# Optimization experiments

Measured on AMD Instinct MI355X. Metric: run time of the kernel, lower is better.

The kernel has to match this reference:

```python
import jax, jax.numpy as jnp
import numpy as np

B, S, D, H = 2, 4096, 512, 8
HD = D // H


def setup_inputs() -> dict:
    key = jax.random.key(0)
    ks = jax.random.split(key, 11)
    s = 1.0 / np.sqrt(D)
    return {
        "queries": jax.random.normal(ks[0], (B, S, D), jnp.float32),
        "keys": jax.random.normal(ks[1], (B, S, D), jnp.float32),
        "values": jax.random.normal(ks[2], (B, S, D), jnp.float32),
        "Wq": jax.random.normal(ks[3], (D, D), jnp.float32) * s,
        "bq": jnp.zeros((D,), jnp.float32),
        "Wk": jax.random.normal(ks[4], (D, D), jnp.float32) * s,
        "bk": jnp.zeros((D,), jnp.float32),
        "Wv": jax.random.normal(ks[5], (D, D), jnp.float32) * s,
        "bv": jnp.zeros((D,), jnp.float32),
        "Wo": jax.random.normal(ks[6], (D, D), jnp.float32) * s,
        "bo": jnp.zeros((D,), jnp.float32),
    }


def reference(queries, keys, values, Wq, bq, Wk, bk, Wv, bv, Wo, bo):
    b = queries.shape[0]
    # Linear projections (torch Linear: x @ W.T + b; here W stored as [in, out])
    q = (queries @ Wq + bq).reshape(b, -1, H, HD)   # [B, Sq, H, HD]
    k = (keys @ Wk + bk).reshape(b, -1, H, HD)       # [B, Sk, H, HD]
    v = (values @ Wv + bv).reshape(b, -1, H, HD)     # [B, Sk, H, HD]
    logits = jnp.einsum('bqhd,bkhd->bhqk', q, k) / jnp.sqrt(jnp.float32(HD))
    attn = jax.nn.softmax(logits, axis=-1)           # [B, H, Sq, Sk]  (dropout_rate=0 -> identity)
    ctx = jnp.einsum('bhqk,bkhd->bqhd', attn, v).reshape(b, -1, H * HD)
    return ctx @ Wo + bo
```

## Files before the change

### kernel.cpp

```cpp
#include <hip/hip_runtime.h>
#include <hip/hip_bf16.h>

constexpr int B_  = 2;
constexpr int S_  = 4096;
constexpr int D_  = 512;
constexpr int H_  = 8;
constexpr int HD_ = 64;
constexpr int M_  = B_ * S_;

typedef __attribute__((ext_vector_type(8))) short short8;
typedef __attribute__((ext_vector_type(4))) float floatx4;
typedef __attribute__((ext_vector_type(16))) float floatx16;

static __device__ __forceinline__ unsigned short f2bf(float f) {
    union { float f; unsigned u; } v; v.f = f;
    unsigned r = v.u + 0x7fffu + ((v.u >> 16) & 1u);
    return (unsigned short)(r >> 16);
}

static __device__ __forceinline__ unsigned pk2bf(float a, float b) {
#if __has_builtin(__builtin_amdgcn_cvt_pk_bf16_f32)
    typedef __attribute__((ext_vector_type(2))) __bf16 bf16x2_t;
    union { bf16x2_t v; unsigned u; } u;
    u.v = __builtin_amdgcn_cvt_pk_bf16_f32(a, b);
    return u.u;
#else
    return (unsigned)f2bf(a) | ((unsigned)f2bf(b) << 16);
#endif
}

static __device__ __forceinline__ void plane32swap(unsigned& x, unsigned& y) {
#if __has_builtin(__builtin_amdgcn_permlane32_swap)
    typedef __attribute__((ext_vector_type(2))) unsigned uint2v;
    uint2v r = __builtin_amdgcn_permlane32_swap(x, y, false, false);
    x = r[0]; y = r[1];
#else
    const bool hi = (threadIdx.x & 32) != 0;
    unsigned xs = __shfl_xor(x, 32), ys = __shfl_xor(y, 32);
    unsigned nx = hi ? ys : x;
    unsigned ny = hi ? y : xs;
    x = nx; y = ny;
#endif
}

#if __has_builtin(__builtin_amdgcn_exp2f)
#define EXP2(x) __builtin_amdgcn_exp2f(x)
#else
#define EXP2(x) exp2f(x)
#endif

#define QSCALE 0.18033688011110204f

static __device__ __forceinline__ void gl_lds16(const void* g, void* l) {
    typedef __attribute__((address_space(1))) const unsigned GU;
    typedef __attribute__((address_space(3))) unsigned LU;
    __builtin_amdgcn_global_load_lds((GU*)g, (LU*)l, 16, 0, 0);
}

__global__ __launch_bounds__(256) void xcast_kernel(
    const float* __restrict__ Xq, const float* __restrict__ Xk, const float* __restrict__ Xv,
    unsigned short* __restrict__ Y) {
    const int z = blockIdx.z;
    const float* X = z == 0 ? Xq : (z == 1 ? Xk : Xv);
    unsigned short* Yz = Y + (size_t)z * M_ * D_;
    const int n8 = M_ * D_ / 8;
    int i = blockIdx.x * 256 + threadIdx.x;
    const int stride = gridDim.x * 256;
    for (; i < n8; i += stride) {
        float4 a = *(const float4*)&X[(size_t)i * 8];
        float4 b = *(const float4*)&X[(size_t)i * 8 + 4];
        union { short8 s; unsigned u[4]; } p;
        p.u[0] = pk2bf(a.x, a.y); p.u[1] = pk2bf(a.z, a.w);
        p.u[2] = pk2bf(b.x, b.y); p.u[3] = pk2bf(b.z, b.w);
        *(short8*)&Yz[(size_t)i * 8] = p.s;
    }
}

__global__ __launch_bounds__(256) void wtrans_kernel(
    const float* __restrict__ Wq, const float* __restrict__ Wk,
    const float* __restrict__ Wv, const float* __restrict__ Wo,
    unsigned short* __restrict__ Tq, unsigned short* __restrict__ Tk,
    unsigned short* __restrict__ Tv, unsigned short* __restrict__ To) {
    const int z = blockIdx.z;
    const float* W = z == 0 ? Wq : (z == 1 ? Wk : (z == 2 ? Wv : Wo));
    unsigned short* Wt = z == 0 ? Tq : (z == 1 ? Tk : (z == 2 ? Tv : To));
    __shared__ float T[64][65];
    const int t = threadIdx.x;
    const int k0 = blockIdx.x * 64, n0 = blockIdx.y * 64;
#pragma unroll
    for (int i = 0; i < 4; ++i) {
        const int flat = t + 256 * i;
        const int kr = flat >> 4, nc = (flat & 15) * 4;
        float4 v = *(const float4*)&W[(size_t)(k0 + kr) * 512 + n0 + nc];
        T[kr][nc] = v.x; T[kr][nc + 1] = v.y; T[kr][nc + 2] = v.z; T[kr][nc + 3] = v.w;
    }
    __syncthreads();
#pragma unroll
    for (int i = 0; i < 4; ++i) {
        const int flat = t + 256 * i;
        const int nr = flat >> 4, kc = (flat & 15) * 4;
        ushort4 o4;
        o4.x = f2bf(T[kc][nr]);     o4.y = f2bf(T[kc + 1][nr]);
        o4.z = f2bf(T[kc + 2][nr]); o4.w = f2bf(T[kc + 3][nr]);
        *(ushort4*)&Wt[(size_t)(n0 + nr) * 512 + k0 + kc] = o4;
    }
}

template <int MODE>
__global__ __launch_bounds__(256, 3) void gemm_kernel(
    const unsigned short* __restrict__ Ab,
    const unsigned short* __restrict__ Wt,
    const float* __restrict__ b0, const float* __restrict__ b1, const float* __restrict__ b2,
    unsigned short* __restrict__ o0, unsigned short* __restrict__ o1,
    unsigned short* __restrict__ o2, float* __restrict__ of) {
    __shared__ unsigned short As[128 * 64];
    __shared__ unsigned short Bs[128 * 64];

    const int tid  = threadIdx.x;
    const int w    = tid >> 6;
    const int lane = tid & 63;
    const int n0   = blockIdx.x * 128;
    const int m0   = blockIdx.y * 128;
    const int lm   = lane & 15;
    const int lq   = lane >> 4;
    const int wm   = (w >> 1) * 64;
    const int wn   = (w & 1) * 64;

    const int z = MODE == 0 ? (n0 >> 9) : 0;
    const unsigned short* A = MODE == 0 ? Ab + (size_t)z * M_ * D_ : Ab;

    const int srow = lane >> 3;
    const int sch  = lane & 7;
    const int ca   = (sch ^ (srow & 7)) * 8;

    floatx4 acc[4][4];
#pragma unroll
    for (int i = 0; i < 4; ++i)
#pragma unroll
        for (int j = 0; j < 4; ++j) acc[i][j] = (floatx4)0.0f;

    for (int kb = 0; kb < 8; ++kb) {
        const int k0 = kb * 64;
        __syncthreads();
#pragma unroll
        for (int it = 0; it < 4; ++it) {
            const int r8 = w * 32 + it * 8;
            gl_lds16(&A [(size_t)(m0 + r8 + srow) * 512 + k0 + ca], &As[r8 * 64]);
            gl_lds16(&Wt[(size_t)(n0 + r8 + srow) * 512 + k0 + ca], &Bs[r8 * 64]);
        }
        __syncthreads();

        short8 af[2][4], bf[2][4];
#pragma unroll
        for (int ks = 0; ks < 2; ++ks)
#pragma unroll
            for (int i = 0; i < 4; ++i) {
                const int cc = ((ks * 4 + lq) ^ (lm & 7)) * 8;
                af[ks][i] = *(const short8*)&As[(wm + i * 16 + lm) * 64 + cc];
                bf[ks][i] = *(const short8*)&Bs[(wn + i * 16 + lm) * 64 + cc];
            }
#pragma unroll
        for (int ks = 0; ks < 2; ++ks)
#pragma unroll
            for (int mi = 0; mi < 4; ++mi)
#pragma unroll
                for (int ni = 0; ni < 4; ++ni)
                    acc[mi][ni] = __builtin_amdgcn_mfma_f32_16x16x32_bf16(
                        af[ks][mi], bf[ks][ni], acc[mi][ni], 0, 0, 0);
    }

    const float* bias = MODE == 0 ? (z == 0 ? b0 : (z == 1 ? b1 : b2)) : b0;
    const float scale = (MODE == 0 && z == 0) ? QSCALE : 1.0f;
    const int nl0 = n0 & 511;

    float bias_n[4];
#pragma unroll
    for (int ni = 0; ni < 4; ++ni) bias_n[ni] = bias[nl0 + wn + ni * 16 + lm];

#pragma unroll
    for (int mi = 0; mi < 4; ++mi) {
#pragma unroll
        for (int ni = 0; ni < 4; ++ni) {
            if (MODE == 1) {
                const int gn = n0 + wn + ni * 16 + lm;
#pragma unroll
                for (int r = 0; r < 4; ++r) {
                    const int gm = m0 + wm + mi * 16 + lq * 4 + r;
                    of[(size_t)gm * 512 + gn] = acc[mi][ni][r] + bias_n[ni];
                }
            } else {
                const int gnl = nl0 + wn + ni * 16 + lm;
                const int h = gnl >> 6, hd = gnl & 63;
                if (z == 2) {
                    const int gm = m0 + wm + mi * 16 + lq * 4;
                    const int b = gm >> 12, s = gm & 4095;
                    union { ushort4 s4; uint2 u; } o4;
                    o4.u.x = pk2bf(acc[mi][ni][0] + bias_n[ni], acc[mi][ni][1] + bias_n[ni]);
                    o4.u.y = pk2bf(acc[mi][ni][2] + bias_n[ni], acc[mi][ni][3] + bias_n[ni]);
                    *(ushort4*)&o2[(((size_t)(b * 8 + h)) * 64 + hd) * 4096 + s] = o4.s4;
                } else {
                    unsigned short* out = z == 0 ? o0 : o1;
#pragma unroll
                    for (int r = 0; r < 4; ++r) {
                        const int gm = m0 + wm + mi * 16 + lq * 4 + r;
                        const int b = gm >> 12, s = gm & 4095;
                        const float vv = (acc[mi][ni][r] + bias_n[ni]) * scale;
                        out[(((size_t)(b * 8 + h)) * 4096 + s) * 64 + hd] = f2bf(vv);
                    }
                }
            }
        }
    }
}

__global__ __launch_bounds__(256, 2) void flash_kernel(
    const unsigned short* __restrict__ Q, const unsigned short* __restrict__ K,
    const unsigned short* __restrict__ Vt, unsigned short* __restrict__ ctx) {
    constexpr int NO = 32;
    __shared__ unsigned short Ks[2][2][64 * 64];
    __shared__ unsigned short Vs[2][2][64 * 64];

    const int tid = threadIdx.x;
    const int w   = tid >> 6;
    const int l   = tid & 63;
    const int lo  = l & 31;
    const int hi  = l >> 5;
    const int lo7 = lo & 7;
    const int q0  = blockIdx.x * 128;
    const int bh  = blockIdx.y;
    const int qw  = q0 + w * 32;

    const size_t base = (size_t)bh * S_ * HD_;
    const unsigned short* Qg = Q + base;
    const unsigned short* Kg = K + base;
    const unsigned short* Vg = Vt + base;

    short8 qf[4];
#pragma unroll
    for (int ds = 0; ds < 4; ++ds)
        qf[ds] = *(const short8*)&Qg[(size_t)(qw + lo) * 64 + ds * 16 + hi * 8];

    short8 ones;
#pragma unroll
    for (int j = 0; j < 8; ++j) ones[j] = (short)0x3F80;

    floatx16 o[2];
    o[0] = (floatx16)0.0f; o[1] = (floatx16)0.0f;
    floatx16 lacc = (floatx16)0.0f;

    const int sr  = tid >> 3, sch = tid & 7;
    const int swz = (sch ^ (sr & 7)) * 8;
    const int sw0 = sr * 64 + swz;
    const int sw1 = (sr + 32) * 64 + swz;

    short8 kr[2][2], vr[2][2];
    auto LOADT2 = [&](int t2) {
#pragma unroll
        for (int j = 0; j < 2; ++j) {
            const int krow = (t2 * 2 + j) * 64;
            kr[j][0] = *(const short8*)&Kg[(size_t)(krow + sr) * 64 + sch * 8];
            kr[j][1] = *(const short8*)&Kg[(size_t)(krow + sr + 32) * 64 + sch * 8];
            vr[j][0] = *(const short8*)&Vg[(size_t)sr * S_ + krow + sch * 8];
            vr[j][1] = *(const short8*)&Vg[(size_t)(sr + 32) * S_ + krow + sch * 8];
        }
    };
    auto WRITE2 = [&](int bb) {
#pragma unroll
        for (int j = 0; j < 2; ++j) {
            *(short8*)&Ks[bb][j][sw0] = kr[j][0];
            *(short8*)&Ks[bb][j][sw1] = kr[j][1];
            *(short8*)&Vs[bb][j][sw0] = vr[j][0];
            *(short8*)&Vs[bb][j][sw1] = vr[j][1];
        }
    };

    LOADT2(0);
    WRITE2(0);
    LOADT2(1);

    for (int it = 0; it < NO; ++it) {
        const int cb = it & 1;
        __syncthreads();
        if (it + 1 < NO) WRITE2(cb ^ 1);
        if (it + 2 < NO) LOADT2(it + 2);

#pragma unroll
        for (int j = 0; j < 2; ++j) {
            const unsigned short* Kc = Ks[cb][j];
            const unsigned short* Vc = Vs[cb][j];

            short8 kf[2][4];
#pragma unroll
            for (int g = 0; g < 2; ++g)
#pragma unroll
                for (int ds = 0; ds < 4; ++ds)
                    kf[g][ds] = *(const short8*)&Kc[(g * 32 + lo) * 64 +
                                                    (((ds * 2 + hi) ^ lo7) * 8)];
            floatx16 s[2];
            s[0] = (floatx16)0.0f; s[1] = (floatx16)0.0f;
            __builtin_amdgcn_s_setprio(1);
#pragma unroll
            for (int g = 0; g < 2; ++g)
#pragma unroll
                for (int ds = 0; ds < 4; ++ds)
                    s[g] = __builtin_amdgcn_mfma_f32_32x32x16_bf16(
                        kf[g][ds], qf[ds], s[g], 0, 0, 0);
            __builtin_amdgcn_s_setprio(0);

#pragma unroll
            for (int g = 0; g < 2; ++g)
#pragma unroll
                for (int r = 0; r < 16; ++r) s[g][r] = EXP2(s[g][r]);

            short8 pa[4];
#pragma unroll
            for (int ks = 0; ks < 4; ++ks) {
                const int g = ks >> 1, kk = (ks & 1) * 8;
                unsigned wa = pk2bf(s[g][kk + 0], s[g][kk + 1]);
                unsigned wb = pk2bf(s[g][kk + 2], s[g][kk + 3]);
                unsigned wc = pk2bf(s[g][kk + 4], s[g][kk + 5]);
                unsigned wd = pk2bf(s[g][kk + 6], s[g][kk + 7]);
                plane32swap(wa, wc);
                plane32swap(wb, wd);
                union { short8 s8; unsigned u[4]; } pk_;
                pk_.u[0] = wa; pk_.u[1] = wb; pk_.u[2] = wc; pk_.u[3] = wd;
                pa[ks] = pk_.s8;
            }

            short8 vf[2][4];
#pragma unroll
            for (int onn = 0; onn < 2; ++onn)
#pragma unroll
                for (int ks = 0; ks < 4; ++ks)
                    vf[onn][ks] = *(const short8*)&Vc[(onn * 32 + lo) * 64 +
                                                      (((ks * 2 + hi) ^ lo7) * 8)];
            __builtin_amdgcn_s_setprio(1);
#pragma unroll
            for (int ks = 0; ks < 4; ++ks) {
                lacc = __builtin_amdgcn_mfma_f32_32x32x16_bf16(pa[ks], ones, lacc, 0, 0, 0);
                o[0] = __builtin_amdgcn_mfma_f32_32x32x16_bf16(pa[ks], vf[0][ks], o[0], 0, 0, 0);
                o[1] = __builtin_amdgcn_mfma_f32_32x32x16_bf16(pa[ks], vf[1][ks], o[1], 0, 0, 0);
            }
            __builtin_amdgcn_s_setprio(0);
        }
    }

    const int b = bh >> 3, h = bh & 7;
#pragma unroll
    for (int r = 0; r < 16; ++r) {
        const float inv = 1.0f / lacc[r];
        const int q = qw + (r & 3) + 8 * (r >> 2) + 4 * hi;
        unsigned short* cp = &ctx[((size_t)(b * S_ + q)) * 512 + h * 64 + lo];
        cp[0]  = f2bf(o[0][r] * inv);
        cp[32] = f2bf(o[1][r] * inv);
    }
}

extern "C" void kernel_launch(void* const* d_in, const int* in_sizes, int n_in,
                              void* d_out, int out_size, void* d_ws, size_t ws_size,
                              hipStream_t stream) {
    const float* queries = (const float*)d_in[0];
    const float* keys    = (const float*)d_in[1];
    const float* values  = (const float*)d_in[2];
    const float* Wq = (const float*)d_in[3];
    const float* bq = (const float*)d_in[4];
    const float* Wk = (const float*)d_in[5];
    const float* bk = (const float*)d_in[6];
    const float* Wv = (const float*)d_in[7];
    const float* bv = (const float*)d_in[8];
    const float* Wo = (const float*)d_in[9];
    const float* bo = (const float*)d_in[10];

    unsigned short* xb    = (unsigned short*)d_ws;
    unsigned short* wsctx = xb;
    unsigned short* wsq   = xb   + (size_t)3 * M_ * D_;
    unsigned short* wsk   = wsq  + (size_t)M_ * D_;
    unsigned short* wsvt  = wsk  + (size_t)M_ * D_;
    unsigned short* wtq   = wsvt + (size_t)M_ * D_;
    unsigned short* wtk   = wtq  + (size_t)D_ * D_;
    unsigned short* wtv   = wtk  + (size_t)D_ * D_;
    unsigned short* wto   = wtv  + (size_t)D_ * D_;

    xcast_kernel<<<dim3(1024, 1, 3), dim3(256), 0, stream>>>(queries, keys, values, xb);
    wtrans_kernel<<<dim3(8, 8, 4), dim3(256), 0, stream>>>(
        Wq, Wk, Wv, Wo, wtq, wtk, wtv, wto);

    gemm_kernel<0><<<dim3(12, 64), dim3(256), 0, stream>>>(
        xb, wtq, bq, bk, bv, wsq, wsk, wsvt, nullptr);

    flash_kernel<<<dim3(S_ / 128, B_ * H_), dim3(256), 0, stream>>>(wsq, wsk, wsvt, wsctx);

    gemm_kernel<1><<<dim3(4, 64), dim3(256), 0, stream>>>(
        wsctx, wto, bo, nullptr, nullptr, nullptr, nullptr, nullptr, (float*)d_out);
}
```

Before: 244.1 us.

## Load K/V fragments directly from global memory, dropping LDS staging

The flash attention kernel no longer stages K and V tiles through double-buffered shared memory with block-wide barriers. Each wave now loads its MFMA operand fragments straight from global memory into registers, with the next K tile prefetched in software. This removes the LDS writes, the LDS reads and the __syncthreads. In exchange, the four waves of a block each fetch the same K/V data separately, so global and L2 traffic rises about fourfold and each fragment load has more latency to hide.

```diff
diff --git a/kernel.cpp b/kernel.cpp
--- a/kernel.cpp
+++ b/kernel.cpp
@@ -216,16 +216,11 @@
 __global__ __launch_bounds__(256, 2) void flash_kernel(
     const unsigned short* __restrict__ Q, const unsigned short* __restrict__ K,
     const unsigned short* __restrict__ Vt, unsigned short* __restrict__ ctx) {
-    constexpr int NO = 32;
-    __shared__ unsigned short Ks[2][2][64 * 64];
-    __shared__ unsigned short Vs[2][2][64 * 64];
-
     const int tid = threadIdx.x;
     const int w   = tid >> 6;
     const int l   = tid & 63;
     const int lo  = l & 31;
     const int hi  = l >> 5;
-    const int lo7 = lo & 7;
     const int q0  = blockIdx.x * 128;
     const int bh  = blockIdx.y;
     const int qw  = q0 + w * 32;
@@ -248,101 +243,74 @@
     o[0] = (floatx16)0.0f; o[1] = (floatx16)0.0f;
     floatx16 lacc = (floatx16)0.0f;
 
-    const int sr  = tid >> 3, sch = tid & 7;
-    const int swz = (sch ^ (sr & 7)) * 8;
-    const int sw0 = sr * 64 + swz;
-    const int sw1 = (sr + 32) * 64 + swz;
-
-    short8 kr[2][2], vr[2][2];
-    auto LOADT2 = [&](int t2) {
-#pragma unroll
-        for (int j = 0; j < 2; ++j) {
-            const int krow = (t2 * 2 + j) * 64;
-            kr[j][0] = *(const short8*)&Kg[(size_t)(krow + sr) * 64 + sch * 8];
-            kr[j][1] = *(const short8*)&Kg[(size_t)(krow + sr + 32) * 64 + sch * 8];
-            vr[j][0] = *(const short8*)&Vg[(size_t)sr * S_ + krow + sch * 8];
-            vr[j][1] = *(const short8*)&Vg[(size_t)(sr + 32) * S_ + krow + sch * 8];
+    auto LOADK = [&](int kt, short8 (&kf)[2][4]) {
+#pragma unroll
+        for (int g = 0; g < 2; ++g)
+#pragma unroll
+            for (int ds = 0; ds < 4; ++ds)
+                kf[g][ds] = *(const short8*)&Kg[(size_t)kt * 4096 + g * 2048 +
+                                                lo * 64 + ds * 16 + hi * 8];
+    };
+    auto LOADV = [&](int kt, short8 (&vf)[2][4]) {
+#pragma unroll
+        for (int onn = 0; onn < 2; ++onn)
+#pragma unroll
+            for (int ks = 0; ks < 4; ++ks)
+                vf[onn][ks] = *(const short8*)&Vg[(size_t)(onn * 32 + lo) * 4096 +
+                                                  kt * 64 + ks * 16 + hi * 8];
+    };
+
+    auto TILE = [&](short8 (&kf)[2][4], short8 (&vf)[2][4]) {
+        floatx16 s[2];
+        s[0] = (floatx16)0.0f; s[1] = (floatx16)0.0f;
+        __builtin_amdgcn_s_setprio(1);
+#pragma unroll
+        for (int g = 0; g < 2; ++g)
+#pragma unroll
+            for (int ds = 0; ds < 4; ++ds)
+                s[g] = __builtin_amdgcn_mfma_f32_32x32x16_bf16(
+                    kf[g][ds], qf[ds], s[g], 0, 0, 0);
+        __builtin_amdgcn_s_setprio(0);
+
+#pragma unroll
+        for (int g = 0; g < 2; ++g)
+#pragma unroll
+            for (int r = 0; r < 16; ++r) s[g][r] = EXP2(s[g][r]);
+
+        short8 pa[4];
+#pragma unroll
+        for (int ks = 0; ks < 4; ++ks) {
+            const int g = ks >> 1, kk = (ks & 1) * 8;
+            unsigned wa = pk2bf(s[g][kk + 0], s[g][kk + 1]);
+            unsigned wb = pk2bf(s[g][kk + 2], s[g][kk + 3]);
+            unsigned wc = pk2bf(s[g][kk + 4], s[g][kk + 5]);
+            unsigned wd = pk2bf(s[g][kk + 6], s[g][kk + 7]);
+            plane32swap(wa, wc);
+            plane32swap(wb, wd);
+            union { short8 s8; unsigned u[4]; } pk_;
+            pk_.u[0] = wa; pk_.u[1] = wb; pk_.u[2] = wc; pk_.u[3] = wd;
+            pa[ks] = pk_.s8;
         }
+
+        __builtin_amdgcn_s_setprio(1);
+#pragma unroll
+        for (int ks = 0; ks < 4; ++ks) {
+            lacc = __builtin_amdgcn_mfma_f32_32x32x16_bf16(pa[ks], ones, lacc, 0, 0, 0);
+            o[0] = __builtin_amdgcn_mfma_f32_32x32x16_bf16(pa[ks], vf[0][ks], o[0], 0, 0, 0);
+            o[1] = __builtin_amdgcn_mfma_f32_32x32x16_bf16(pa[ks], vf[1][ks], o[1], 0, 0, 0);
+        }
+        __builtin_amdgcn_s_setprio(0);
     };
-    auto WRITE2 = [&](int bb) {
-#pragma unroll
-        for (int j = 0; j < 2; ++j) {
-            *(short8*)&Ks[bb][j][sw0] = kr[j][0];
-            *(short8*)&Ks[bb][j][sw1] = kr[j][1];
-            *(short8*)&Vs[bb][j][sw0] = vr[j][0];
-            *(short8*)&Vs[bb][j][sw1] = vr[j][1];
-        }
-    };
-
-    LOADT2(0);
-    WRITE2(0);
-    LOADT2(1);
-
-    for (int it = 0; it < NO; ++it) {
-        const int cb = it & 1;
-        __syncthreads();
-        if (it + 1 < NO) WRITE2(cb ^ 1);
-        if (it + 2 < NO) LOADT2(it + 2);
-
-#pragma unroll
-        for (int j = 0; j < 2; ++j) {
-            const unsigned short* Kc = Ks[cb][j];
-            const unsigned short* Vc = Vs[cb][j];
-
-            short8 kf[2][4];
-#pragma unroll
-            for (int g = 0; g < 2; ++g)
-#pragma unroll
-                for (int ds = 0; ds < 4; ++ds)
-                    kf[g][ds] = *(const short8*)&Kc[(g * 32 + lo) * 64 +
-                                                    (((ds * 2 + hi) ^ lo7) * 8)];
-            floatx16 s[2];
-            s[0] = (floatx16)0.0f; s[1] = (floatx16)0.0f;
-            __builtin_amdgcn_s_setprio(1);
-#pragma unroll
-            for (int g = 0; g < 2; ++g)
-#pragma unroll
-                for (int ds = 0; ds < 4; ++ds)
-                    s[g] = __builtin_amdgcn_mfma_f32_32x32x16_bf16(
-                        kf[g][ds], qf[ds], s[g], 0, 0, 0);
-            __builtin_amdgcn_s_setprio(0);
-
-#pragma unroll
-            for (int g = 0; g < 2; ++g)
-#pragma unroll
-                for (int r = 0; r < 16; ++r) s[g][r] = EXP2(s[g][r]);
-
-            short8 pa[4];
-#pragma unroll
-            for (int ks = 0; ks < 4; ++ks) {
-                const int g = ks >> 1, kk = (ks & 1) * 8;
-                unsigned wa = pk2bf(s[g][kk + 0], s[g][kk + 1]);
-                unsigned wb = pk2bf(s[g][kk + 2], s[g][kk + 3]);
-                unsigned wc = pk2bf(s[g][kk + 4], s[g][kk + 5]);
-                unsigned wd = pk2bf(s[g][kk + 6], s[g][kk + 7]);
-                plane32swap(wa, wc);
-                plane32swap(wb, wd);
-                union { short8 s8; unsigned u[4]; } pk_;
-                pk_.u[0] = wa; pk_.u[1] = wb; pk_.u[2] = wc; pk_.u[3] = wd;
-                pa[ks] = pk_.s8;
-            }
-
-            short8 vf[2][4];
-#pragma unroll
-            for (int onn = 0; onn < 2; ++onn)
-#pragma unroll
-                for (int ks = 0; ks < 4; ++ks)
-                    vf[onn][ks] = *(const short8*)&Vc[(onn * 32 + lo) * 64 +
-                                                      (((ks * 2 + hi) ^ lo7) * 8)];
-            __builtin_amdgcn_s_setprio(1);
-#pragma unroll
-            for (int ks = 0; ks < 4; ++ks) {
-                lacc = __builtin_amdgcn_mfma_f32_32x32x16_bf16(pa[ks], ones, lacc, 0, 0, 0);
-                o[0] = __builtin_amdgcn_mfma_f32_32x32x16_bf16(pa[ks], vf[0][ks], o[0], 0, 0, 0);
-                o[1] = __builtin_amdgcn_mfma_f32_32x32x16_bf16(pa[ks], vf[1][ks], o[1], 0, 0, 0);
-            }
-            __builtin_amdgcn_s_setprio(0);
-        }
+
+    short8 kfA[2][4], kfB[2][4], vfc[2][4];
+    LOADK(0, kfA);
+    for (int kt = 0; kt < 64; kt += 2) {
+        LOADV(kt, vfc);
+        LOADK(kt + 1, kfB);
+        TILE(kfA, vfc);
+        LOADV(kt + 1, vfc);
+        if (kt + 2 < 64) LOADK(kt + 2, kfA);
+        TILE(kfB, vfc);
     }
 
     const int b = bh >> 3, h = bh & 7;
```

Result: slower. 373.8 us (+53.2%).
